# Kernel tuning notes

Hardware: AMD Instinct MI355X
Metric: run time of the kernel (lower is better)

The kernel has to match this reference:

```python
import jax, jax.numpy as jnp
import numpy as np

B, D = 64, 65536   # batch, num default boxes
NEG_POS = 3        # negative:positive mining ratio (init arg)


def _bce_with_logits(x, t):
    # numerically stable elementwise BCE-with-logits (matches torch)
    return jnp.maximum(x, 0.0) - x * t + jnp.log1p(jnp.exp(-jnp.abs(x)))


def _smooth_l1(d):
    ad = jnp.abs(d)
    return jnp.where(ad < 1.0, 0.5 * d * d, ad - 0.5)


def setup_inputs() -> dict:
    key = jax.random.key(0)
    k1, k2, k3, k4 = jax.random.split(key, 4)
    loc_data = jax.random.normal(k1, (B, D, 4), dtype=jnp.float32)
    conf_data = jax.random.normal(k2, (B, D, 1), dtype=jnp.float32)
    loc_t = jax.random.normal(k3, (B, D, 4), dtype=jnp.float32)
    conf_t = (jax.random.uniform(k4, (B, D)) < 0.02).astype(jnp.int32)
    return {"loc_data": loc_data, "conf_data": conf_data,
            "loc_t": loc_t, "conf_t": conf_t}


def reference(loc_data, conf_data, loc_t, conf_t):
    pos = conf_t > 0                                  # [B, D]
    num_pos = pos.sum(axis=1, keepdims=True)          # [B, 1]

    # ---- localization loss: smooth-L1 mean over positive box coords ----
    pf = pos[:, :, None].astype(loc_data.dtype)       # [B, D, 1]
    sl1 = _smooth_l1(loc_data - loc_t) * pf           # [B, D, 4]
    n_loc_elems = pf.sum() * 4.0                      # masked-gather -> mean
    loss_l = sl1.sum() / n_loc_elems

    # ---- confidence loss with hard negative mining ----
    logits = conf_data[:, :, 0]                       # [B, D]
    bce = _bce_with_logits(logits, conf_t.astype(logits.dtype))
    bce_neg = jnp.where(pos, 0.0, bce)                # zero-out positives
    # double argsort -> per-row rank of each element's loss (descending)
    loss_idx = jnp.argsort(-bce_neg, axis=1)          # [B, D]
    idx_rank = jnp.argsort(loss_idx, axis=1)          # [B, D]
    num_neg = jnp.minimum(num_pos * NEG_POS, D)       # [B, 1]
    neg = idx_rank < num_neg                          # top-k hardest negatives
    sel = (pos | neg).astype(logits.dtype)            # [B, D]
    loss_c = (bce * sel).sum() / sel.sum()            # mean over selected

    N = num_pos.sum().astype(logits.dtype)
    return (loss_l / N, loss_c / N)
```

## Files before the change

kernel.cpp:

```cpp
#include <hip/hip_runtime.h>
#include <stdint.h>


#define B_ 64
#define D_ 65536
#define NEGPOS 3
#define BPR 16
#define CHUNK (D_ / BPR)
#define XC 1.25f
#define CAPC 16384
#define NREG 32

#define OFF_SL1      0
#define OFF_BCEP     8
#define OFF_NEGSUM   16
#define OFF_NUMPOS   528
#define OFF_CANDCNT  784
#define OFF_POSCNT   1040
#define ZERO_BYTES   1056
#define OFF_KSEL     1056
#define OFF_CAND     2048
#define OFF_POSL     (2048 + 64 * CAPC * 4)

__device__ __forceinline__ float softplus_f(float x) {
    return fmaxf(x, 0.0f) + log1pf(expf(-fabsf(x)));
}

__device__ __forceinline__ unsigned sortkey(float x) {
    unsigned u = __float_as_uint(x);
    return (u & 0x80000000u) ? ~u : (u | 0x80000000u);
}
__device__ __forceinline__ float unsortkey(unsigned s) {
    unsigned u = (s & 0x80000000u) ? (s & 0x7FFFFFFFu) : ~s;
    return __uint_as_float(u);
}

__device__ __forceinline__ float smooth_l1_4(float4 a, float4 b) {
    float s = 0.0f, d, ad;
    d = a.x - b.x; ad = fabsf(d); s += (ad < 1.0f) ? 0.5f * d * d : ad - 0.5f;
    d = a.y - b.y; ad = fabsf(d); s += (ad < 1.0f) ? 0.5f * d * d : ad - 0.5f;
    d = a.z - b.z; ad = fabsf(d); s += (ad < 1.0f) ? 0.5f * d * d : ad - 0.5f;
    d = a.w - b.w; ad = fabsf(d); s += (ad < 1.0f) ? 0.5f * d * d : ad - 0.5f;
    return s;
}

__device__ __forceinline__ double wredD(double v) {
#pragma unroll
    for (int o = 32; o > 0; o >>= 1) v += __shfl_down(v, o, 64);
    return v;
}
__device__ __forceinline__ int wredI(int v) {
#pragma unroll
    for (int o = 32; o > 0; o >>= 1) v += __shfl_down(v, o, 64);
    return v;
}

__device__ __forceinline__ void wave_push_f(bool pred, float val,
                                            unsigned* cnt, float* buf) {
    unsigned long long m = __ballot(pred);
    if (m == 0ull) return;
    const int lane = threadIdx.x & 63;
    const int leader = (int)(__ffsll((long long)m) - 1);
    unsigned base = 0;
    if (lane == leader) base = atomicAdd(cnt, (unsigned)__popcll(m));
    base = __shfl(base, leader, 64);
    if (pred) buf[base + __popcll(m & ((1ull << lane) - 1ull))] = val;
}
__device__ __forceinline__ void wave_push_u(bool pred, unsigned val,
                                            unsigned* cnt, unsigned* buf) {
    unsigned long long m = __ballot(pred);
    if (m == 0ull) return;
    const int lane = threadIdx.x & 63;
    const int leader = (int)(__ffsll((long long)m) - 1);
    unsigned base = 0;
    if (lane == leader) base = atomicAdd(cnt, (unsigned)__popcll(m));
    base = __shfl(base, leader, 64);
    if (pred) buf[base + __popcll(m & ((1ull << lane) - 1ull))] = val;
}

__global__ void __launch_bounds__(256)
mbl_k1(const float* __restrict__ conf, const int* __restrict__ conft,
       unsigned char* __restrict__ ws)
{
    __shared__ float lcand[CHUNK];
    __shared__ unsigned lpos[CHUNK];
    __shared__ unsigned ccnt_s, pcnt_s, cbase_s, pbase_s;
    __shared__ double wbce[4];
    __shared__ int wnp[4];
    if (threadIdx.x == 0) { ccnt_s = 0; pcnt_s = 0; }
    __syncthreads();

    const int row = blockIdx.x / BPR;
    const int chunk = blockIdx.x % BPR;
    const int base = row * D_ + chunk * CHUNK;
    const float4* c4 = (const float4*)(conf + base);
    const int4*   t4 = (const int4*)(conft + base);

    float4 xv[4]; int4 tv[4];
#pragma unroll
    for (int it = 0; it < 4; it++) {
        const int g = threadIdx.x + it * 256;
        xv[it] = c4[g];
        tv[it] = t4[g];
    }

    double bcep = 0.0;
    int np = 0;
#pragma unroll
    for (int it = 0; it < 4; it++) {
        const int g = threadIdx.x + it * 256;
#pragma unroll
        for (int c = 0; c < 4; c++) {
            float x = (c == 0) ? xv[it].x : (c == 1) ? xv[it].y : (c == 2) ? xv[it].z : xv[it].w;
            int   t = (c == 0) ? tv[it].x : (c == 1) ? tv[it].y : (c == 2) ? tv[it].z : tv[it].w;
            const bool isp = (t > 0);
            if (isp) { np++; bcep += (double)(softplus_f(x) - x); }
            wave_push_u(isp, (unsigned)(base + g * 4 + c), &pcnt_s, lpos);
            wave_push_f(!isp && (x >= XC), x, &ccnt_s, lcand);
        }
    }
    __syncthreads();

    if (threadIdx.x == 0) {
        cbase_s = atomicAdd((unsigned*)(ws + OFF_CANDCNT) + row, ccnt_s);
        pbase_s = atomicAdd((unsigned*)(ws + OFF_POSCNT), pcnt_s);
    }
    __syncthreads();
    {
        float* cand = (float*)(ws + OFF_CAND) + row * CAPC;
        const unsigned n = ccnt_s, b0 = cbase_s;
        for (unsigned i = threadIdx.x; i < n; i += 256) {
            unsigned p = b0 + i;
            if (p < CAPC) cand[p] = lcand[i];
        }
        unsigned* posl = (unsigned*)(ws + OFF_POSL);
        const unsigned m = pcnt_s, p0 = pbase_s;
        for (unsigned i = threadIdx.x; i < m; i += 256)
            posl[p0 + i] = lpos[i];
    }

    double bc = wredD(bcep);
    int n = wredI(np);
    const int lane = threadIdx.x & 63, wid = threadIdx.x >> 6;
    if (lane == 0) { wbce[wid] = bc; wnp[wid] = n; }
    __syncthreads();
    if (threadIdx.x == 0) {
        atomicAdd((double*)(ws + OFF_BCEP), wbce[0] + wbce[1] + wbce[2] + wbce[3]);
        atomicAdd((int*)(ws + OFF_NUMPOS) + row, wnp[0] + wnp[1] + wnp[2] + wnp[3]);
    }
}

__global__ void __launch_bounds__(256)
mbl_kpos(const float4* __restrict__ loc4, const float4* __restrict__ loct4,
         unsigned char* __restrict__ ws)
{
    __shared__ double wr[4];
    const unsigned cnt = *(const unsigned*)(ws + OFF_POSCNT);
    const unsigned* posl = (const unsigned*)(ws + OFF_POSL);
    double sl1 = 0.0;
    for (unsigned i = blockIdx.x * 256 + threadIdx.x; i < cnt; i += gridDim.x * 256) {
        unsigned e = posl[i];
        sl1 += (double)smooth_l1_4(loc4[e], loct4[e]);
    }
    double t = wredD(sl1);
    const int lane = threadIdx.x & 63, wid = threadIdx.x >> 6;
    if (lane == 0) wr[wid] = t;
    __syncthreads();
    if (threadIdx.x == 0)
        atomicAdd((double*)(ws + OFF_SL1), wr[0] + wr[1] + wr[2] + wr[3]);
}

__device__ __forceinline__ int blockSumI(int v, int* sh) {
    int w = wredI(v);
    const int lane = threadIdx.x & 63, wid = threadIdx.x >> 6;
    __syncthreads();
    if (lane == 0) sh[wid] = w;
    __syncthreads();
    return sh[0] + sh[1] + sh[2] + sh[3];
}

__global__ void __launch_bounds__(256)
mbl_ksel(const float* __restrict__ conf, const int* __restrict__ conft,
         unsigned char* __restrict__ ws)
{
    __shared__ int shI[4];
    __shared__ double wr[4];

    const int row = blockIdx.x;
    const int np = ((const int*)(ws + OFF_NUMPOS))[row];
    long long k = (long long)np * NEGPOS;
    if (k > D_) k = D_;
    long long negs = (long long)D_ - np;
    if (k > negs) k = negs;
    if (threadIdx.x == 0) ((int*)(ws + OFF_KSEL))[row] = (int)k;
    if (k <= 0) return;

    const unsigned nc = ((const unsigned*)(ws + OFF_CANDCNT))[row];
    const bool fb = (nc > (unsigned)(NREG * 256)) || (nc > (unsigned)CAPC) ||
                    ((long long)nc < k);
    const float* cand = (const float*)(ws + OFF_CAND) + row * CAPC;
    const float* rowc = conf + row * D_;
    const int*   rowt = conft + row * D_;

    unsigned lo = 0u, hi = 0xFFFFFFFFu;
    int rem;
    unsigned Tkey;

    if (!fb) {
        const int n = (int)nc;
        unsigned keys[NREG];
#pragma unroll
        for (int j = 0; j < NREG; j++) {
            const int i = j * 256 + (int)threadIdx.x;
            keys[j] = (i < n) ? sortkey(cand[i]) : 0u;
        }
        for (int it = 0; it < 32; it++) {
            const unsigned mid = lo + ((hi - lo) >> 1);
            int c = 0;
#pragma unroll
            for (int j = 0; j < NREG; j++) c += (keys[j] > mid) ? 1 : 0;
            const int tot = blockSumI(c, shI);
            if ((long long)tot >= k) lo = mid; else hi = mid;
        }
        Tkey = hi;
        int c = 0;
#pragma unroll
        for (int j = 0; j < NREG; j++) c += (keys[j] > Tkey) ? 1 : 0;
        rem = (int)(k - (long long)blockSumI(c, shI));

        double acc = 0.0;
#pragma unroll
        for (int j = 0; j < NREG; j++)
            if (keys[j] > Tkey) acc += (double)softplus_f(unsortkey(keys[j]));
        double t = wredD(acc);
        const int lane = threadIdx.x & 63, wid = threadIdx.x >> 6;
        if (lane == 0) wr[wid] = t;
        __syncthreads();
        if (threadIdx.x == 0)
            ((double*)(ws + OFF_NEGSUM))[row] =
                wr[0] + wr[1] + wr[2] + wr[3] +
                (double)rem * (double)softplus_f(unsortkey(Tkey));
    } else {
        for (int it = 0; it < 32; it++) {
            const unsigned mid = lo + ((hi - lo) >> 1);
            int c = 0;
            for (int i = threadIdx.x; i < D_; i += 256)
                if (rowt[i] <= 0 && sortkey(rowc[i]) > mid) c++;
            const int tot = blockSumI(c, shI);
            if ((long long)tot >= k) lo = mid; else hi = mid;
        }
        Tkey = hi;
        int c = 0;
        double acc = 0.0;
        for (int i = threadIdx.x; i < D_; i += 256) {
            if (rowt[i] <= 0) {
                float x = rowc[i];
                if (sortkey(x) > Tkey) { c++; acc += (double)softplus_f(x); }
            }
        }
        rem = (int)(k - (long long)blockSumI(c, shI));
        double t = wredD(acc);
        const int lane = threadIdx.x & 63, wid = threadIdx.x >> 6;
        if (lane == 0) wr[wid] = t;
        __syncthreads();
        if (threadIdx.x == 0)
            ((double*)(ws + OFF_NEGSUM))[row] =
                wr[0] + wr[1] + wr[2] + wr[3] +
                (double)rem * (double)softplus_f(unsortkey(Tkey));
    }
}

__global__ void __launch_bounds__(64)
mbl_k5(unsigned char* __restrict__ ws, float* __restrict__ out)
{
    const int t = threadIdx.x;
    int np = ((const int*)(ws + OFF_NUMPOS))[t];
    int k  = ((const int*)(ws + OFF_KSEL))[t];
    double ns = ((const double*)(ws + OFF_NEGSUM))[t];
    int npT = wredI(np);
    int kT  = wredI(k);
    double nsT = wredD(ns);
    if (t == 0) {
        double Np = (double)npT;
        double sl1  = *((const double*)(ws + OFF_SL1));
        double bcep = *((const double*)(ws + OFF_BCEP));
        double out0 = (Np > 0.0) ? (sl1 / (4.0 * Np)) / Np : 0.0;
        double denom = Np + (double)kT;
        double out1 = (Np > 0.0 && denom > 0.0) ? ((bcep + nsT) / denom) / Np : 0.0;
        out[0] = (float)out0;
        out[1] = (float)out1;
    }
}

extern "C" void kernel_launch(void* const* d_in, const int* in_sizes, int n_in,
                              void* d_out, int out_size, void* d_ws, size_t ws_size,
                              hipStream_t stream)
{
    const float4* loc4  = (const float4*)d_in[0];
    const float*  conf  = (const float*)d_in[1];
    const float4* loct4 = (const float4*)d_in[2];
    const int*    conft = (const int*)d_in[3];
    unsigned char* ws = (unsigned char*)d_ws;
    float* out = (float*)d_out;

    hipMemsetAsync(ws, 0, ZERO_BYTES, stream);
    mbl_k1<<<dim3(B_ * BPR), dim3(256), 0, stream>>>(conf, conft, ws);
    mbl_kpos<<<dim3(512), dim3(256), 0, stream>>>(loc4, loct4, ws);
    mbl_ksel<<<dim3(B_), dim3(256), 0, stream>>>(conf, conft, ws);
    mbl_k5<<<dim3(1), dim3(64), 0, stream>>>(ws, out);
}
```

Before: 206.1 us.

## Fuse positive smooth-L1 into first pass, replace atomics with per-block partials

The positive-box smooth-L1 gather moves into the first kernel, which removes the separate mbl_kpos launch and the global positive-index list. Wave ballots and atomics used for compaction are replaced by a counting pass plus a packed prefix scan that gives deterministic local offsets. Each block now writes its partial sums and counts into fixed slots instead of using global atomics, which also removes the memset. The selection kernel rebuilds per-row candidate offsets from 16 segments and finds each element's segment by binary search, adding some index arithmetic in exchange for fewer launches and no atomic contention.

```diff
diff --git a/kernel.cpp b/kernel.cpp
--- a/kernel.cpp
+++ b/kernel.cpp
@@ -6,21 +6,19 @@
 #define D_ 65536
 #define NEGPOS 3
 #define BPR 16
+#define NBLK (B_ * BPR)
 #define CHUNK (D_ / BPR)
 #define XC 1.25f
 #define CAPC 16384
 #define NREG 32
 
-#define OFF_SL1      0
-#define OFF_BCEP     8
-#define OFF_NEGSUM   16
-#define OFF_NUMPOS   528
-#define OFF_CANDCNT  784
-#define OFF_POSCNT   1040
-#define ZERO_BYTES   1056
-#define OFF_KSEL     1056
-#define OFF_CAND     2048
-#define OFF_POSL     (2048 + 64 * CAPC * 4)
+#define OFF_SL1P     0
+#define OFF_BCEP     8192
+#define OFF_NP       16384
+#define OFF_CC       20480
+#define OFF_NEGSUM   24576
+#define OFF_KSEL     25088
+#define OFF_CAND     32768
 
 __device__ __forceinline__ float softplus_f(float x) {
     return fmaxf(x, 0.0f) + log1pf(expf(-fabsf(x)));
@@ -55,46 +53,21 @@
     return v;
 }
 
-__device__ __forceinline__ void wave_push_f(bool pred, float val,
-                                            unsigned* cnt, float* buf) {
-    unsigned long long m = __ballot(pred);
-    if (m == 0ull) return;
-    const int lane = threadIdx.x & 63;
-    const int leader = (int)(__ffsll((long long)m) - 1);
-    unsigned base = 0;
-    if (lane == leader) base = atomicAdd(cnt, (unsigned)__popcll(m));
-    base = __shfl(base, leader, 64);
-    if (pred) buf[base + __popcll(m & ((1ull << lane) - 1ull))] = val;
-}
-__device__ __forceinline__ void wave_push_u(bool pred, unsigned val,
-                                            unsigned* cnt, unsigned* buf) {
-    unsigned long long m = __ballot(pred);
-    if (m == 0ull) return;
-    const int lane = threadIdx.x & 63;
-    const int leader = (int)(__ffsll((long long)m) - 1);
-    unsigned base = 0;
-    if (lane == leader) base = atomicAdd(cnt, (unsigned)__popcll(m));
-    base = __shfl(base, leader, 64);
-    if (pred) buf[base + __popcll(m & ((1ull << lane) - 1ull))] = val;
-}
-
 __global__ void __launch_bounds__(256)
-mbl_k1(const float* __restrict__ conf, const int* __restrict__ conft,
+mbl_k1(const float4* __restrict__ loc4, const float* __restrict__ conf,
+       const float4* __restrict__ loct4, const int* __restrict__ conft,
        unsigned char* __restrict__ ws)
 {
     __shared__ float lcand[CHUNK];
-    __shared__ unsigned lpos[CHUNK];
-    __shared__ unsigned ccnt_s, pcnt_s, cbase_s, pbase_s;
-    __shared__ double wbce[4];
-    __shared__ int wnp[4];
-    if (threadIdx.x == 0) { ccnt_s = 0; pcnt_s = 0; }
-    __syncthreads();
-
-    const int row = blockIdx.x / BPR;
-    const int chunk = blockIdx.x % BPR;
-    const int base = row * D_ + chunk * CHUNK;
+    __shared__ unsigned short lpos[CHUNK];
+    __shared__ unsigned wtot[4];
+    __shared__ double wr[8];
+
+    const int block = blockIdx.x;
+    const int base = block * CHUNK;
     const float4* c4 = (const float4*)(conf + base);
     const int4*   t4 = (const int4*)(conft + base);
+    const int lane = threadIdx.x & 63, wid = threadIdx.x >> 6;
 
     float4 xv[4]; int4 tv[4];
 #pragma unroll
@@ -105,69 +78,66 @@
     }
 
     double bcep = 0.0;
-    int np = 0;
+    unsigned cntc = 0, cntp = 0;
 #pragma unroll
     for (int it = 0; it < 4; it++) {
-        const int g = threadIdx.x + it * 256;
 #pragma unroll
         for (int c = 0; c < 4; c++) {
             float x = (c == 0) ? xv[it].x : (c == 1) ? xv[it].y : (c == 2) ? xv[it].z : xv[it].w;
             int   t = (c == 0) ? tv[it].x : (c == 1) ? tv[it].y : (c == 2) ? tv[it].z : tv[it].w;
-            const bool isp = (t > 0);
-            if (isp) { np++; bcep += (double)(softplus_f(x) - x); }
-            wave_push_u(isp, (unsigned)(base + g * 4 + c), &pcnt_s, lpos);
-            wave_push_f(!isp && (x >= XC), x, &ccnt_s, lcand);
-        }
-    }
-    __syncthreads();
-
+            if (t > 0) { cntp++; bcep += (double)(softplus_f(x) - x); }
+            else if (x >= XC) cntc++;
+        }
+    }
+
+    unsigned pk = (cntc << 16) | cntp;
+    unsigned incl = pk;
+#pragma unroll
+    for (int o = 1; o < 64; o <<= 1) {
+        unsigned v = __shfl_up(incl, o, 64);
+        if (lane >= o) incl += v;
+    }
+    unsigned excl = incl - pk;
+    if (lane == 63) wtot[wid] = incl;
+    __syncthreads();
+    unsigned wbase = 0;
+    for (int w = 0; w < wid; w++) wbase += wtot[w];
+    const unsigned tot = wtot[0] + wtot[1] + wtot[2] + wtot[3];
+    const unsigned totc = tot >> 16, totp = tot & 0xFFFFu;
+    unsigned offc = (excl >> 16) + (wbase >> 16);
+    unsigned offp = (excl & 0xFFFFu) + (wbase & 0xFFFFu);
+
+#pragma unroll
+    for (int it = 0; it < 4; it++) {
+#pragma unroll
+        for (int c = 0; c < 4; c++) {
+            float x = (c == 0) ? xv[it].x : (c == 1) ? xv[it].y : (c == 2) ? xv[it].z : xv[it].w;
+            int   t = (c == 0) ? tv[it].x : (c == 1) ? tv[it].y : (c == 2) ? tv[it].z : tv[it].w;
+            const int li = (threadIdx.x + it * 256) * 4 + c;
+            if (t > 0) lpos[offp++] = (unsigned short)li;
+            else if (x >= XC) lcand[offc++] = x;
+        }
+    }
+    __syncthreads();
+
+    float* seg = (float*)(ws + OFF_CAND) + (size_t)block * CHUNK;
+    for (unsigned i = threadIdx.x; i < totc; i += 256) seg[i] = lcand[i];
+
+    double sl1 = 0.0;
+    for (unsigned i = threadIdx.x; i < totp; i += 256) {
+        const int e = base + (int)lpos[i];
+        sl1 += (double)smooth_l1_4(loc4[e], loct4[e]);
+    }
+
+    double s1 = wredD(sl1), s2 = wredD(bcep);
+    if (lane == 0) { wr[wid] = s1; wr[4 + wid] = s2; }
+    __syncthreads();
     if (threadIdx.x == 0) {
-        cbase_s = atomicAdd((unsigned*)(ws + OFF_CANDCNT) + row, ccnt_s);
-        pbase_s = atomicAdd((unsigned*)(ws + OFF_POSCNT), pcnt_s);
-    }
-    __syncthreads();
-    {
-        float* cand = (float*)(ws + OFF_CAND) + row * CAPC;
-        const unsigned n = ccnt_s, b0 = cbase_s;
-        for (unsigned i = threadIdx.x; i < n; i += 256) {
-            unsigned p = b0 + i;
-            if (p < CAPC) cand[p] = lcand[i];
-        }
-        unsigned* posl = (unsigned*)(ws + OFF_POSL);
-        const unsigned m = pcnt_s, p0 = pbase_s;
-        for (unsigned i = threadIdx.x; i < m; i += 256)
-            posl[p0 + i] = lpos[i];
-    }
-
-    double bc = wredD(bcep);
-    int n = wredI(np);
-    const int lane = threadIdx.x & 63, wid = threadIdx.x >> 6;
-    if (lane == 0) { wbce[wid] = bc; wnp[wid] = n; }
-    __syncthreads();
-    if (threadIdx.x == 0) {
-        atomicAdd((double*)(ws + OFF_BCEP), wbce[0] + wbce[1] + wbce[2] + wbce[3]);
-        atomicAdd((int*)(ws + OFF_NUMPOS) + row, wnp[0] + wnp[1] + wnp[2] + wnp[3]);
-    }
-}
-
-__global__ void __launch_bounds__(256)
-mbl_kpos(const float4* __restrict__ loc4, const float4* __restrict__ loct4,
-         unsigned char* __restrict__ ws)
-{
-    __shared__ double wr[4];
-    const unsigned cnt = *(const unsigned*)(ws + OFF_POSCNT);
-    const unsigned* posl = (const unsigned*)(ws + OFF_POSL);
-    double sl1 = 0.0;
-    for (unsigned i = blockIdx.x * 256 + threadIdx.x; i < cnt; i += gridDim.x * 256) {
-        unsigned e = posl[i];
-        sl1 += (double)smooth_l1_4(loc4[e], loct4[e]);
-    }
-    double t = wredD(sl1);
-    const int lane = threadIdx.x & 63, wid = threadIdx.x >> 6;
-    if (lane == 0) wr[wid] = t;
-    __syncthreads();
-    if (threadIdx.x == 0)
-        atomicAdd((double*)(ws + OFF_SL1), wr[0] + wr[1] + wr[2] + wr[3]);
+        ((double*)(ws + OFF_SL1P))[block] = wr[0] + wr[1] + wr[2] + wr[3];
+        ((double*)(ws + OFF_BCEP))[block] = wr[4] + wr[5] + wr[6] + wr[7];
+        ((unsigned*)(ws + OFF_NP))[block] = totp;
+        ((unsigned*)(ws + OFF_CC))[block] = totc;
+    }
 }
 
 __device__ __forceinline__ int blockSumI(int v, int* sh) {
@@ -183,36 +153,61 @@
 mbl_ksel(const float* __restrict__ conf, const int* __restrict__ conft,
          unsigned char* __restrict__ ws)
 {
+    __shared__ unsigned segoff[BPR + 1];
     __shared__ int shI[4];
     __shared__ double wr[4];
 
     const int row = blockIdx.x;
-    const int np = ((const int*)(ws + OFF_NUMPOS))[row];
+    const unsigned* cc = (const unsigned*)(ws + OFF_CC) + row * BPR;
+    const unsigned* npb = (const unsigned*)(ws + OFF_NP) + row * BPR;
+
+    if (threadIdx.x == 0) {
+        unsigned o = 0;
+        int np = 0;
+#pragma unroll
+        for (int s = 0; s < BPR; s++) { segoff[s] = o; o += cc[s]; np += (int)npb[s]; }
+        segoff[BPR] = o;
+        shI[0] = np;
+    }
+    __syncthreads();
+    const int np = shI[0];
+    const unsigned n = segoff[BPR];
     long long k = (long long)np * NEGPOS;
     if (k > D_) k = D_;
     long long negs = (long long)D_ - np;
     if (k > negs) k = negs;
     if (threadIdx.x == 0) ((int*)(ws + OFF_KSEL))[row] = (int)k;
-    if (k <= 0) return;
-
-    const unsigned nc = ((const unsigned*)(ws + OFF_CANDCNT))[row];
-    const bool fb = (nc > (unsigned)(NREG * 256)) || (nc > (unsigned)CAPC) ||
-                    ((long long)nc < k);
-    const float* cand = (const float*)(ws + OFF_CAND) + row * CAPC;
+    if (k <= 0) {
+        if (threadIdx.x == 0) ((double*)(ws + OFF_NEGSUM))[row] = 0.0;
+        return;
+    }
+    __syncthreads();
+
+    const bool fb = ((long long)n < k) || (n > (unsigned)(NREG * 256)) ||
+                    (n > (unsigned)CAPC);
+    const float* cand = (const float*)(ws + OFF_CAND);
     const float* rowc = conf + row * D_;
     const int*   rowt = conft + row * D_;
-
+    const int lane = threadIdx.x & 63, wid = threadIdx.x >> 6;
     unsigned lo = 0u, hi = 0xFFFFFFFFu;
     int rem;
     unsigned Tkey;
 
     if (!fb) {
-        const int n = (int)nc;
         unsigned keys[NREG];
 #pragma unroll
         for (int j = 0; j < NREG; j++) {
-            const int i = j * 256 + (int)threadIdx.x;
-            keys[j] = (i < n) ? sortkey(cand[i]) : 0u;
+            const unsigned g = (unsigned)(j * 256) + threadIdx.x;
+            unsigned key = 0u;
+            if (g < n) {
+                int s = 0;
+#pragma unroll
+                for (int st = 8; st > 0; st >>= 1)
+                    if (s + st <= BPR && segoff[s + st] <= g) s += st;
+                const unsigned idx = g - segoff[s];
+                key = sortkey(cand[(size_t)(row * BPR + s) * CHUNK + idx]);
+            }
+            keys[j] = key;
         }
         for (int it = 0; it < 32; it++) {
             const unsigned mid = lo + ((hi - lo) >> 1);
@@ -233,7 +228,6 @@
         for (int j = 0; j < NREG; j++)
             if (keys[j] > Tkey) acc += (double)softplus_f(unsortkey(keys[j]));
         double t = wredD(acc);
-        const int lane = threadIdx.x & 63, wid = threadIdx.x >> 6;
         if (lane == 0) wr[wid] = t;
         __syncthreads();
         if (threadIdx.x == 0)
@@ -260,7 +254,6 @@
         }
         rem = (int)(k - (long long)blockSumI(c, shI));
         double t = wredD(acc);
-        const int lane = threadIdx.x & 63, wid = threadIdx.x >> 6;
         if (lane == 0) wr[wid] = t;
         __syncthreads();
         if (threadIdx.x == 0)
@@ -270,23 +263,38 @@
     }
 }
 
-__global__ void __launch_bounds__(64)
+__global__ void __launch_bounds__(256)
 mbl_k5(unsigned char* __restrict__ ws, float* __restrict__ out)
 {
-    const int t = threadIdx.x;
-    int np = ((const int*)(ws + OFF_NUMPOS))[t];
-    int k  = ((const int*)(ws + OFF_KSEL))[t];
-    double ns = ((const double*)(ws + OFF_NEGSUM))[t];
-    int npT = wredI(np);
-    int kT  = wredI(k);
-    double nsT = wredD(ns);
-    if (t == 0) {
-        double Np = (double)npT;
-        double sl1  = *((const double*)(ws + OFF_SL1));
-        double bcep = *((const double*)(ws + OFF_BCEP));
-        double out0 = (Np > 0.0) ? (sl1 / (4.0 * Np)) / Np : 0.0;
-        double denom = Np + (double)kT;
-        double out1 = (Np > 0.0 && denom > 0.0) ? ((bcep + nsT) / denom) / Np : 0.0;
+    __shared__ double wrA[4], wrB[4], wrC[4];
+    __shared__ int shN[4], shK[4];
+    const double* sl1p = (const double*)(ws + OFF_SL1P);
+    const double* bcep = (const double*)(ws + OFF_BCEP);
+    const unsigned* npb = (const unsigned*)(ws + OFF_NP);
+    const int* ksel = (const int*)(ws + OFF_KSEL);
+    const double* ns = (const double*)(ws + OFF_NEGSUM);
+
+    double a = 0.0, b = 0.0, c = 0.0;
+    int n = 0, kk = 0;
+    for (int i = threadIdx.x; i < NBLK; i += 256) {
+        a += sl1p[i]; b += bcep[i]; n += (int)npb[i];
+    }
+    if (threadIdx.x < 64) { kk = ksel[threadIdx.x]; c = ns[threadIdx.x]; }
+
+    double ra = wredD(a), rb = wredD(b), rc = wredD(c);
+    int rn = wredI(n), rk = wredI(kk);
+    const int lane = threadIdx.x & 63, wid = threadIdx.x >> 6;
+    if (lane == 0) { wrA[wid] = ra; wrB[wid] = rb; wrC[wid] = rc; shN[wid] = rn; shK[wid] = rk; }
+    __syncthreads();
+    if (threadIdx.x == 0) {
+        double SL1 = wrA[0] + wrA[1] + wrA[2] + wrA[3];
+        double BCE = wrB[0] + wrB[1] + wrB[2] + wrB[3];
+        double NSUM = wrC[0] + wrC[1] + wrC[2] + wrC[3];
+        double Np = (double)(shN[0] + shN[1] + shN[2] + shN[3]);
+        double Kt = (double)(shK[0] + shK[1] + shK[2] + shK[3]);
+        double out0 = (Np > 0.0) ? (SL1 / (4.0 * Np)) / Np : 0.0;
+        double denom = Np + Kt;
+        double out1 = (Np > 0.0 && denom > 0.0) ? ((BCE + NSUM) / denom) / Np : 0.0;
         out[0] = (float)out0;
         out[1] = (float)out1;
     }
@@ -303,9 +311,7 @@
     unsigned char* ws = (unsigned char*)d_ws;
     float* out = (float*)d_out;
 
-    hipMemsetAsync(ws, 0, ZERO_BYTES, stream);
-    mbl_k1<<<dim3(B_ * BPR), dim3(256), 0, stream>>>(conf, conft, ws);
-    mbl_kpos<<<dim3(512), dim3(256), 0, stream>>>(loc4, loct4, ws);
+    mbl_k1<<<dim3(NBLK), dim3(256), 0, stream>>>(loc4, conf, loct4, conft, ws);
     mbl_ksel<<<dim3(B_), dim3(256), 0, stream>>>(conf, conft, ws);
-    mbl_k5<<<dim3(1), dim3(64), 0, stream>>>(ws, out);
-}
+    mbl_k5<<<dim3(1), dim3(256), 0, stream>>>(ws, out);
+}
```

Result: faster. 195.4 us (-5.2%).
